# Optimization experiments

Hardware: AMD Instinct MI355X
Metric: run time of the kernel (lower is better)

Reference implementation:

```python
import jax, jax.numpy as jnp
import numpy as np

B, L, D, H = 2, 2048, 2048, 16
HD = D // H  # head_dim = 128
EPS = 1e-5


def setup_inputs() -> dict:
    key = jax.random.key(0)
    ks = jax.random.split(key, 5)
    return {
        "x": jax.random.normal(ks[0], (B, L, D), dtype=jnp.float32),
        "Wq": jax.random.normal(ks[1], (D, D), dtype=jnp.float32) * (D ** -0.5),
        "Wk": jax.random.normal(ks[2], (D, D), dtype=jnp.float32) * (D ** -0.5),
        "Wv": jax.random.normal(ks[3], (D, D), dtype=jnp.float32) * (D ** -0.5),
        "gamma_logit": jax.random.normal(ks[4], (H,), dtype=jnp.float32),
        "gn_weight": jnp.ones((D,), dtype=jnp.float32),
        "gn_bias": jnp.zeros((D,), dtype=jnp.float32),
    }


def reference(x, Wq, Wk, Wv, gamma_logit, gn_weight, gn_bias):
    scale = HD ** -0.5
    # projections (torch Linear: y = x @ W.T)
    Q = jnp.einsum('bld,ed->ble', x, Wq).reshape(B, L, H, HD).transpose(0, 2, 1, 3)
    K = jnp.einsum('bld,ed->ble', x, Wk).reshape(B, L, H, HD).transpose(0, 2, 1, 3)
    V = jnp.einsum('bld,ed->ble', x, Wv).reshape(B, L, H, HD).transpose(0, 2, 1, 3)
    # causal exponential decay matrix D[h,i,j] = gamma_h^(i-j), lower-triangular
    pos = jnp.arange(L)
    dist = jnp.abs(pos[None, :] - pos[:, None]).astype(jnp.float32)  # [L,L]
    gamma = jax.nn.sigmoid(gamma_logit)  # [H]
    Dmat = jnp.tril(gamma[:, None, None] ** dist[None, :, :])  # [H,L,L]
    # decayed linear attention (no softmax)
    attn = jnp.einsum('bhid,bhjd->bhij', Q, K) * scale * Dmat[None]
    out = jnp.einsum('bhij,bhje->bhie', attn, V)  # [B,H,L,HD]
    out = out.transpose(0, 2, 1, 3)  # [B,L,H,HD]
    # GroupNorm: channels=D, groups=H, spatial=L -> normalize per (b,h) over (L,HD)
    mean = out.mean(axis=(1, 3), keepdims=True)
    var = out.var(axis=(1, 3), keepdims=True)
    y = (out - mean) * jax.lax.rsqrt(var + EPS)
    y = y * gn_weight.reshape(1, 1, H, HD) + gn_bias.reshape(1, 1, H, HD)
    return y.reshape(B, L, D)
```

## Files before the change

kernel.cpp:

```cpp
#include <hip/hip_runtime.h>
#include <hip/hip_bf16.h>
#include <math.h>

#define B_  2
#define L_  2048
#define D_  2048
#define H_  16
#define HD_ 128
#define EPS_ 1e-5f

typedef __attribute__((ext_vector_type(8)))  short short8;
typedef __attribute__((ext_vector_type(4)))  float f32x4;
typedef __attribute__((ext_vector_type(16))) float f32x16;

static __device__ inline unsigned short bfb(float x) {
    __hip_bfloat16 h = __float2bfloat16(x);
    unsigned short s;
    __builtin_memcpy(&s, &h, 2);
    return s;
}
static __device__ inline unsigned pk2(float a, float b) {
    return (unsigned)bfb(a) | ((unsigned)bfb(b) << 16);
}

static __device__ __forceinline__ void gld_lds16(const void* g, void* l) {
    __builtin_amdgcn_global_load_lds(
        (const __attribute__((address_space(1))) unsigned int*)g,
        (__attribute__((address_space(3))) unsigned int*)l,
        16, 0, 0);
}

#define XN4 2097152
#define WN4 1048576
#define TOT4 (XN4 + 3 * WN4)

__global__ __launch_bounds__(256) void cast4_kernel(
    const float* __restrict__ x,  const float* __restrict__ Wq,
    const float* __restrict__ Wk, const float* __restrict__ Wv,
    __hip_bfloat16* __restrict__ dst)
{
    int i = blockIdx.x * 256 + threadIdx.x;
    const int st = gridDim.x * 256;
    for (; i < TOT4; i += st) {
        const float* s;
        int off;
        if (i < XN4)                { s = x;  off = i; }
        else if (i < XN4 + WN4)     { s = Wq; off = i - XN4; }
        else if (i < XN4 + 2 * WN4) { s = Wk; off = i - XN4 - WN4; }
        else                        { s = Wv; off = i - XN4 - 2 * WN4; }
        float4 v = ((const float4*)s)[off];
        uint2 r;
        r.x = pk2(v.x, v.y);
        r.y = pk2(v.z, v.w);
        ((uint2*)dst)[i] = r;
    }
}

__global__ __launch_bounds__(256) void proj_bf16(
    const __hip_bfloat16* __restrict__ X,
    const __hip_bfloat16* __restrict__ Wqb, const __hip_bfloat16* __restrict__ Wkb,
    const __hip_bfloat16* __restrict__ Wvb,
    __hip_bfloat16* __restrict__ Qo, __hip_bfloat16* __restrict__ Ko,
    __hip_bfloat16* __restrict__ Vt)
{
    const __hip_bfloat16* W = (blockIdx.z == 0) ? Wqb : (blockIdx.z == 1 ? Wkb : Wvb);
    __hip_bfloat16*       O = (blockIdx.z == 0) ? Qo  : (blockIdx.z == 1 ? Ko  : Vt);

    __shared__ __align__(16) char Al[128 * 64 * 2];
    __shared__ __align__(16) char Bl[128 * 64 * 2];

    const int t  = threadIdx.x;
    const int w  = t >> 6, l = t & 63;
    const int li = l & 15, hi4 = l >> 4;
    const int wr = w >> 1, wc = w & 1;
    const int m0 = blockIdx.y * 128;
    const int n0 = blockIdx.x * 128;

    const int srow = l >> 3;
    const int scol = ((l & 7) ^ (l >> 3)) * 8;

    f32x4 acc[4][4];
    #pragma unroll
    for (int i = 0; i < 4; ++i)
        #pragma unroll
        for (int j = 0; j < 4; ++j)
            #pragma unroll
            for (int r = 0; r < 4; ++r) acc[i][j][r] = 0.f;

    for (int k0 = 0; k0 < D_; k0 += 64) {
        if (k0) __syncthreads();
        #pragma unroll
        for (int c = 0; c < 4; ++c) {
            const int chunk = w * 4 + c;
            const int row   = chunk * 8 + srow;
            gld_lds16(X + (size_t)(m0 + row) * D_ + k0 + scol, Al + chunk * 1024);
            gld_lds16(W + (size_t)(n0 + row) * D_ + k0 + scol, Bl + chunk * 1024);
        }
        __syncthreads();

        #pragma unroll
        for (int s = 0; s < 2; ++s) {
            const int cbA = (s * 64 + hi4 * 16) ^ ((li & 7) << 4);
            short8 af[4], bf[4];
            #pragma unroll
            for (int mi = 0; mi < 4; ++mi)
                af[mi] = *(const short8*)(Al + (wr * 64 + mi * 16 + li) * 128 + cbA);
            #pragma unroll
            for (int ni = 0; ni < 4; ++ni)
                bf[ni] = *(const short8*)(Bl + (wc * 64 + ni * 16 + li) * 128 + cbA);
            #pragma unroll
            for (int mi = 0; mi < 4; ++mi)
                #pragma unroll
                for (int ni = 0; ni < 4; ++ni)
                    acc[mi][ni] = __builtin_amdgcn_mfma_f32_16x16x32_bf16(
                        af[mi], bf[ni], acc[mi][ni], 0, 0, 0);
        }
    }

    if (blockIdx.z == 2) {
        #pragma unroll
        for (int mi = 0; mi < 4; ++mi) {
            #pragma unroll
            for (int ni = 0; ni < 4; ++ni) {
                const int n     = n0 + wc * 64 + ni * 16 + li;
                const int mbase = m0 + wr * 64 + mi * 16 + hi4 * 4;
                const int b = mbase >> 11, ml = mbase & (L_ - 1);
                uint2 w2;
                w2.x = pk2(acc[mi][ni][0], acc[mi][ni][1]);
                w2.y = pk2(acc[mi][ni][2], acc[mi][ni][3]);
                *(uint2*)&O[((size_t)b * (H_ * HD_) + n) * L_ + ml] = w2;
            }
        }
    } else {
        #pragma unroll
        for (int mi = 0; mi < 4; ++mi) {
            #pragma unroll
            for (int ni = 0; ni < 4; ++ni) {
                const int n  = n0 + wc * 64 + ni * 16 + li;
                const int h  = n >> 7, hd = n & (HD_ - 1);
                #pragma unroll
                for (int r = 0; r < 4; ++r) {
                    const int m = m0 + wr * 64 + mi * 16 + hi4 * 4 + r;
                    const int b = m >> 11, ml = m & (L_ - 1);
                    O[((size_t)(b * H_ + h) * L_ + ml) * HD_ + hd] =
                        __float2bfloat16(acc[mi][ni][r]);
                }
            }
        }
    }
}

__global__ __launch_bounds__(256) void retn_kernel(
    const __hip_bfloat16* __restrict__ Qb, const __hip_bfloat16* __restrict__ Kb,
    const __hip_bfloat16* __restrict__ VT, const float* __restrict__ gl,
    float* __restrict__ out)
{
    const int bid = blockIdx.x;
    const int mm  = bid >> 5;
    const int m   = (mm < 8) ? (15 - mm) : (mm - 8);
    const int bh  = bid & 31;
    const int b   = bh >> 4, h = bh & (H_ - 1);
    const int t   = threadIdx.x;
    const int w   = t >> 6, l = t & 63;
    const int li  = l & 31, hi = l >> 5;

    const float gamma = 1.f / (1.f + __expf(-gl[h]));
    const float lg2   = __log2f(gamma);
    const float scale = 0.08838834764831845f;

    __shared__ __align__(16) char Klds[32768];
    __shared__ __align__(16) char Vlds[32768];

    const size_t base = (size_t)bh * (L_ * HD_);
    const __hip_bfloat16* VTg = VT + (size_t)bh * (HD_ * L_);
    const int i0 = m * 128 + w * 32;

    short8 qf[8];
    {
        const __hip_bfloat16* qrow = Qb + base + (size_t)(i0 + li) * HD_;
        #pragma unroll
        for (int s = 0; s < 8; ++s)
            qf[s] = *(const short8*)(qrow + s * 16 + hi * 8);
    }

    float df[16];
    #pragma unroll
    for (int r = 0; r < 16; ++r) {
        const int jl = (r & 3) + 8 * (r >> 2) + 4 * hi;
        df[r] = exp2f(lg2 * (float)(li - jl));
    }

    f32x16 acc[4];
    #pragma unroll
    for (int c = 0; c < 4; ++c)
        #pragma unroll
        for (int r = 0; r < 16; ++r) acc[c][r] = 0.f;

    const int srow4 = l >> 4;
    const int sslot = l & 15;

    for (int gj = 0; gj <= m * 128; gj += 128) {
        __syncthreads();
        #pragma unroll
        for (int cc = 0; cc < 8; ++cc) {
            const int c  = w * 8 + cc;
            const int r  = c * 4 + srow4;
            const int sc = ((sslot ^ (r & 15)) * 8);
            gld_lds16(Kb + base + (size_t)(gj + r) * HD_ + sc, Klds + c * 1024);
            gld_lds16(VTg + (size_t)r * L_ + gj + sc,          Vlds + c * 1024);
        }
        __syncthreads();

        const int tmax = ((i0 - gj) >> 5) < 3 ? ((i0 - gj) >> 5) : 3;
        for (int jt = 0; jt <= tmax; ++jt) {
            const int j0 = gj + jt * 32;

            f32x16 c;
            #pragma unroll
            for (int r = 0; r < 16; ++r) c[r] = 0.f;
            #pragma unroll
            for (int s = 0; s < 8; ++s) {
                short8 kf = *(const short8*)(Klds + (jt * 32 + li) * 256 +
                                             (((s * 2 + hi) ^ (li & 15)) << 4));
                c = __builtin_amdgcn_mfma_f32_32x32x16_bf16(kf, qf[s], c, 0, 0, 0);
            }

            float p[16];
            const float bt = exp2f(lg2 * (float)(i0 - j0)) * scale;
            if (j0 == i0) {
                #pragma unroll
                for (int r = 0; r < 16; ++r) {
                    const int jl = (r & 3) + 8 * (r >> 2) + 4 * hi;
                    p[r] = (jl <= li) ? c[r] * (df[r] * bt) : 0.f;
                }
            } else {
                #pragma unroll
                for (int r = 0; r < 16; ++r) p[r] = c[r] * (df[r] * bt);
            }

            #pragma unroll
            for (int sl = 0; sl < 2; ++sl) {
                const int o = sl * 8;
                unsigned pk01 = pk2(p[o + 0], p[o + 1]);
                unsigned pk23 = pk2(p[o + 2], p[o + 3]);
                unsigned pk45 = pk2(p[o + 4], p[o + 5]);
                unsigned pk67 = pk2(p[o + 6], p[o + 7]);
                unsigned x01 = (unsigned)__shfl_xor((int)pk01, 32);
                unsigned x23 = (unsigned)__shfl_xor((int)pk23, 32);
                unsigned x45 = (unsigned)__shfl_xor((int)pk45, 32);
                unsigned x67 = (unsigned)__shfl_xor((int)pk67, 32);
                union { short8 v; unsigned u[4]; } pf;
                pf.u[0] = hi ? x45 : pk01;
                pf.u[1] = hi ? x67 : pk23;
                pf.u[2] = hi ? pk45 : x01;
                pf.u[3] = hi ? pk67 : x23;
                #pragma unroll
                for (int cch = 0; cch < 4; ++cch) {
                    short8 vf = *(const short8*)(Vlds + (cch * 32 + li) * 256 +
                                 (((jt * 4 + sl * 2 + hi) ^ (li & 15)) << 4));
                    acc[cch] = __builtin_amdgcn_mfma_f32_32x32x16_bf16(
                        pf.v, vf, acc[cch], 0, 0, 0);
                }
            }
        }
    }

    #pragma unroll
    for (int cch = 0; cch < 4; ++cch) {
        #pragma unroll
        for (int r = 0; r < 16; ++r) {
            const int row = (r & 3) + 8 * (r >> 2) + 4 * hi;
            out[(size_t)(b * L_ + i0 + row) * D_ + h * HD_ + cch * 32 + li] =
                acc[cch][r];
        }
    }
}

__global__ __launch_bounds__(256) void gn_stats(
    const float* __restrict__ out, float2* __restrict__ part)
{
    const int bh = blockIdx.x, sl = blockIdx.y;
    const int b = bh >> 4, h = bh & (H_ - 1);
    const int t = threadIdx.x;

    float s = 0.f, sq = 0.f;
    #pragma unroll 4
    for (int it = 0; it < 16; ++it) {
        const int n  = it * 256 + t;
        const int ll = n >> 5, d4 = n & 31;
        float4 v = *(const float4*)&out[(size_t)(b * L_ + sl * 128 + ll) * D_ + h * HD_ + d4 * 4];
        s  += v.x + v.y + v.z + v.w;
        sq += v.x * v.x + v.y * v.y + v.z * v.z + v.w * v.w;
    }
    #pragma unroll
    for (int off = 32; off > 0; off >>= 1) {
        s  += __shfl_down(s, off);
        sq += __shfl_down(sq, off);
    }
    __shared__ float rs[4], rq[4];
    const int wv = t >> 6, lane = t & 63;
    if (lane == 0) { rs[wv] = s; rq[wv] = sq; }
    __syncthreads();
    if (t == 0)
        part[bh * 16 + sl] = make_float2(rs[0] + rs[1] + rs[2] + rs[3],
                                         rq[0] + rq[1] + rq[2] + rq[3]);
}

__global__ __launch_bounds__(256) void gn_apply(
    float* __restrict__ out, const float2* __restrict__ part,
    const float* __restrict__ gw, const float* __restrict__ gb)
{
    const int bh = blockIdx.x, sl = blockIdx.y;
    const int b = bh >> 4, h = bh & (H_ - 1);
    const int t = threadIdx.x;

    float S = 0.f, SQ = 0.f;
    #pragma unroll
    for (int i = 0; i < 16; ++i) {
        float2 p = part[bh * 16 + i];
        S += p.x; SQ += p.y;
    }
    const float inv  = 1.f / (float)(L_ * HD_);
    const float mean = S * inv;
    float var = SQ * inv - mean * mean;
    if (var < 0.f) var = 0.f;
    const float rstd = rsqrtf(var + EPS_);

    #pragma unroll
    for (int it = 0; it < 4; ++it) {
        const int n  = it * 256 + t;
        const int ll = n >> 5, d4 = n & 31;
        const size_t idx = (size_t)(b * L_ + sl * 32 + ll) * D_ + h * HD_ + d4 * 4;
        float4 v = *(const float4*)&out[idx];
        const float4 w4 = *(const float4*)&gw[h * HD_ + d4 * 4];
        const float4 b4 = *(const float4*)&gb[h * HD_ + d4 * 4];
        v.x = (v.x - mean) * rstd * w4.x + b4.x;
        v.y = (v.y - mean) * rstd * w4.y + b4.y;
        v.z = (v.z - mean) * rstd * w4.z + b4.z;
        v.w = (v.w - mean) * rstd * w4.w + b4.w;
        *(float4*)&out[idx] = v;
    }
}

extern "C" void kernel_launch(void* const* d_in, const int* in_sizes, int n_in,
                              void* d_out, int out_size, void* d_ws, size_t ws_size,
                              hipStream_t stream) {
    const float* x  = (const float*)d_in[0];
    const float* Wq = (const float*)d_in[1];
    const float* Wk = (const float*)d_in[2];
    const float* Wv = (const float*)d_in[3];
    const float* gl = (const float*)d_in[4];
    const float* gw = (const float*)d_in[5];
    const float* gb = (const float*)d_in[6];
    float* out = (float*)d_out;

    __hip_bfloat16* ws = (__hip_bfloat16*)d_ws;
    __hip_bfloat16* xb  = ws;
    __hip_bfloat16* Wqb = xb  + 8388608;
    __hip_bfloat16* Wkb = Wqb + 4194304;
    __hip_bfloat16* Wvb = Wkb + 4194304;
    __hip_bfloat16* Qbf = Wvb + 4194304;
    __hip_bfloat16* Kbf = Qbf + 8388608;
    __hip_bfloat16* VTb = Kbf + 8388608;
    float2* part = (float2*)(VTb + 8388608);

    cast4_kernel<<<2048, 256, 0, stream>>>(x, Wq, Wk, Wv, xb);

    dim3 pgrid(D_ / 128, (B_ * L_) / 128, 3);
    proj_bf16<<<pgrid, 256, 0, stream>>>(xb, Wqb, Wkb, Wvb, Qbf, Kbf, VTb);

    retn_kernel<<<dim3(512), 256, 0, stream>>>(Qbf, Kbf, VTb, gl, out);

    gn_stats<<<dim3(32, 16), 256, 0, stream>>>(out, part);
    gn_apply<<<dim3(32, 64), 256, 0, stream>>>(out, part, gw, gb);
}
```

Before: 224.9 us.

## Rewrite projection GEMM with 4-stage LDS pipeline, 256x128 tiles, fused QKV weights

```diff
diff --git a/kernel.cpp b/kernel.cpp
--- a/kernel.cpp
+++ b/kernel.cpp
@@ -56,28 +56,39 @@
     }
 }
 
-__global__ __launch_bounds__(256) void proj_bf16(
+#define NT_ 64
+
+__global__ __launch_bounds__(512, 2) void proj_fused(
     const __hip_bfloat16* __restrict__ X,
-    const __hip_bfloat16* __restrict__ Wqb, const __hip_bfloat16* __restrict__ Wkb,
-    const __hip_bfloat16* __restrict__ Wvb,
+    const __hip_bfloat16* __restrict__ Wc,
     __hip_bfloat16* __restrict__ Qo, __hip_bfloat16* __restrict__ Ko,
-    __hip_bfloat16* __restrict__ Vt)
+    __hip_bfloat16* __restrict__ VT)
 {
-    const __hip_bfloat16* W = (blockIdx.z == 0) ? Wqb : (blockIdx.z == 1 ? Wkb : Wvb);
-    __hip_bfloat16*       O = (blockIdx.z == 0) ? Qo  : (blockIdx.z == 1 ? Ko  : Vt);
-
-    __shared__ __align__(16) char Al[128 * 64 * 2];
-    __shared__ __align__(16) char Bl[128 * 64 * 2];
-
-    const int t  = threadIdx.x;
-    const int w  = t >> 6, l = t & 63;
-    const int li = l & 15, hi4 = l >> 4;
-    const int wr = w >> 1, wc = w & 1;
-    const int m0 = blockIdx.y * 128;
-    const int n0 = blockIdx.x * 128;
-
-    const int srow = l >> 3;
-    const int scol = ((l & 7) ^ (l >> 3)) * 8;
+    __shared__ __align__(16) char lds[98304];
+
+    const int t   = threadIdx.x;
+    const int w   = t >> 6, l = t & 63;
+    const int li  = l & 15, hi4 = l >> 4;
+    const int wr  = w >> 1, wcn = w & 1;
+
+    const int wg = ((blockIdx.x & 7) * 96) + (blockIdx.x >> 3);
+    const int m0 = (wg & 15) * 256;
+    const int n0 = (wg >> 4) * 128;
+
+    const int srow   = 16 * w + 2 * (l >> 3) + ((l & 7) >> 2);
+    const int kslot8 = ((l & 3) ^ ((l >> 3) & 3)) * 8;
+
+    const int fro  = (li >> 1) * 128 + (li & 1) * 64 + ((hi4 ^ ((li >> 1) & 3)) << 4);
+    const int aoff = wr  * 4096 + fro;
+    const int boff = wcn * 4096 + fro;
+
+    auto STAGE = [&](int tt) {
+        char* Ab = lds + (tt & 3) * 24576;
+        const size_t kc = (size_t)(tt * 32) + kslot8;
+        gld_lds16(X  + (size_t)(m0 + srow) * D_ + kc,       Ab + w * 1024);
+        gld_lds16(X  + (size_t)(m0 + 128 + srow) * D_ + kc, Ab + 8192 + w * 1024);
+        gld_lds16(Wc + (size_t)(n0 + srow) * D_ + kc,       Ab + 16384 + w * 1024);
+    };
 
     f32x4 acc[4][4];
     #pragma unroll
@@ -87,56 +98,73 @@
             #pragma unroll
             for (int r = 0; r < 4; ++r) acc[i][j][r] = 0.f;
 
-    for (int k0 = 0; k0 < D_; k0 += 64) {
-        if (k0) __syncthreads();
-        #pragma unroll
-        for (int c = 0; c < 4; ++c) {
-            const int chunk = w * 4 + c;
-            const int row   = chunk * 8 + srow;
-            gld_lds16(X + (size_t)(m0 + row) * D_ + k0 + scol, Al + chunk * 1024);
-            gld_lds16(W + (size_t)(n0 + row) * D_ + k0 + scol, Bl + chunk * 1024);
-        }
-        __syncthreads();
-
-        #pragma unroll
-        for (int s = 0; s < 2; ++s) {
-            const int cbA = (s * 64 + hi4 * 16) ^ ((li & 7) << 4);
-            short8 af[4], bf[4];
+    STAGE(0); STAGE(1); STAGE(2);
+    asm volatile("s_waitcnt vmcnt(6)" ::: "memory");
+    __builtin_amdgcn_s_barrier();
+
+    for (int tq = 0; tq < NT_ / 4; ++tq) {
+        #pragma unroll
+        for (int j = 0; j < 4; ++j) {
+            const int tt = tq * 4 + j;
+            const char* Ab = lds + j * 24576;
+            const char* Bb = Ab + 16384;
+
+            short8 af[4], bfr[4];
             #pragma unroll
             for (int mi = 0; mi < 4; ++mi)
-                af[mi] = *(const short8*)(Al + (wr * 64 + mi * 16 + li) * 128 + cbA);
+                af[mi] = *(const short8*)(Ab + aoff + mi * 1024);
             #pragma unroll
             for (int ni = 0; ni < 4; ++ni)
-                bf[ni] = *(const short8*)(Bl + (wc * 64 + ni * 16 + li) * 128 + cbA);
+                bfr[ni] = *(const short8*)(Bb + boff + ni * 1024);
+
+            if (tt <= NT_ - 4) STAGE(tt + 3);
+
+            if (tt <= NT_ - 4)      asm volatile("s_waitcnt vmcnt(6)" ::: "memory");
+            else if (tt == NT_ - 3) asm volatile("s_waitcnt vmcnt(3)" ::: "memory");
+            else if (tt == NT_ - 2) asm volatile("s_waitcnt vmcnt(0)" ::: "memory");
+
+            __builtin_amdgcn_sched_barrier(0);
+            __builtin_amdgcn_s_barrier();
+            __builtin_amdgcn_sched_barrier(0);
+
+            __builtin_amdgcn_s_setprio(1);
             #pragma unroll
             for (int mi = 0; mi < 4; ++mi)
                 #pragma unroll
                 for (int ni = 0; ni < 4; ++ni)
                     acc[mi][ni] = __builtin_amdgcn_mfma_f32_16x16x32_bf16(
-                        af[mi], bf[ni], acc[mi][ni], 0, 0, 0);
-        }
-    }
-
-    if (blockIdx.z == 2) {
+                        af[mi], bfr[ni], acc[mi][ni], 0, 0, 0);
+            __builtin_amdgcn_s_setprio(0);
+
+            __builtin_amdgcn_sched_barrier(0);
+            __builtin_amdgcn_s_barrier();
+            __builtin_amdgcn_sched_barrier(0);
+        }
+    }
+
+    const int zsel = n0 >> 11;
+    const int np   = n0 & (D_ - 1);
+    if (zsel == 2) {
         #pragma unroll
         for (int mi = 0; mi < 4; ++mi) {
             #pragma unroll
             for (int ni = 0; ni < 4; ++ni) {
-                const int n     = n0 + wc * 64 + ni * 16 + li;
+                const int n     = np + wcn * 64 + ni * 16 + li;
                 const int mbase = m0 + wr * 64 + mi * 16 + hi4 * 4;
                 const int b = mbase >> 11, ml = mbase & (L_ - 1);
                 uint2 w2;
                 w2.x = pk2(acc[mi][ni][0], acc[mi][ni][1]);
                 w2.y = pk2(acc[mi][ni][2], acc[mi][ni][3]);
-                *(uint2*)&O[((size_t)b * (H_ * HD_) + n) * L_ + ml] = w2;
+                *(uint2*)&VT[((size_t)b * D_ + n) * L_ + ml] = w2;
             }
         }
     } else {
+        __hip_bfloat16* O = zsel ? Ko : Qo;
         #pragma unroll
         for (int mi = 0; mi < 4; ++mi) {
             #pragma unroll
             for (int ni = 0; ni < 4; ++ni) {
-                const int n  = n0 + wc * 64 + ni * 16 + li;
+                const int n  = np + wcn * 64 + ni * 16 + li;
                 const int h  = n >> 7, hd = n & (HD_ - 1);
                 #pragma unroll
                 for (int r = 0; r < 4; ++r) {
@@ -366,8 +394,7 @@
 
     cast4_kernel<<<2048, 256, 0, stream>>>(x, Wq, Wk, Wv, xb);
 
-    dim3 pgrid(D_ / 128, (B_ * L_) / 128, 3);
-    proj_bf16<<<pgrid, 256, 0, stream>>>(xb, Wqb, Wkb, Wvb, Qbf, Kbf, VTb);
+    proj_fused<<<dim3(768), 512, 0, stream>>>(xb, Wqb, Qbf, Kbf, VTb);
 
     retn_kernel<<<dim3(512), 256, 0, stream>>>(Qbf, Kbf, VTb, gl, out);
 
```

Result: no change. 229.1 us (+1.9%).

## Widen projection tiles over concatenated weights and fuse GN stats into retention

Applied to the files above, without the earlier changes.

```diff
diff --git a/kernel.cpp b/kernel.cpp
--- a/kernel.cpp
+++ b/kernel.cpp
@@ -56,32 +56,30 @@
     }
 }
 
-__global__ __launch_bounds__(256) void proj_bf16(
+__global__ __launch_bounds__(256, 3) void proj_wide(
     const __hip_bfloat16* __restrict__ X,
-    const __hip_bfloat16* __restrict__ Wqb, const __hip_bfloat16* __restrict__ Wkb,
-    const __hip_bfloat16* __restrict__ Wvb,
+    const __hip_bfloat16* __restrict__ Wc,
     __hip_bfloat16* __restrict__ Qo, __hip_bfloat16* __restrict__ Ko,
-    __hip_bfloat16* __restrict__ Vt)
+    __hip_bfloat16* __restrict__ VT)
 {
-    const __hip_bfloat16* W = (blockIdx.z == 0) ? Wqb : (blockIdx.z == 1 ? Wkb : Wvb);
-    __hip_bfloat16*       O = (blockIdx.z == 0) ? Qo  : (blockIdx.z == 1 ? Ko  : Vt);
-
-    __shared__ __align__(16) char Al[128 * 64 * 2];
+    __shared__ __align__(16) char Al[256 * 64 * 2];
     __shared__ __align__(16) char Bl[128 * 64 * 2];
 
     const int t  = threadIdx.x;
     const int w  = t >> 6, l = t & 63;
     const int li = l & 15, hi4 = l >> 4;
-    const int wr = w >> 1, wc = w & 1;
-    const int m0 = blockIdx.y * 128;
-    const int n0 = blockIdx.x * 128;
+    const int wr = w >> 1, wcn = w & 1;
+
+    const int wg  = (blockIdx.x & 7) * 96 + (blockIdx.x >> 3);
+    const int m0  = (wg & 15) * 256;
+    const int n0g = (wg >> 4) * 128;
 
     const int srow = l >> 3;
     const int scol = ((l & 7) ^ (l >> 3)) * 8;
 
-    f32x4 acc[4][4];
-    #pragma unroll
-    for (int i = 0; i < 4; ++i)
+    f32x4 acc[8][4];
+    #pragma unroll
+    for (int i = 0; i < 8; ++i)
         #pragma unroll
         for (int j = 0; j < 4; ++j)
             #pragma unroll
@@ -90,57 +88,64 @@
     for (int k0 = 0; k0 < D_; k0 += 64) {
         if (k0) __syncthreads();
         #pragma unroll
-        for (int c = 0; c < 4; ++c) {
-            const int chunk = w * 4 + c;
-            const int row   = chunk * 8 + srow;
-            gld_lds16(X + (size_t)(m0 + row) * D_ + k0 + scol, Al + chunk * 1024);
-            gld_lds16(W + (size_t)(n0 + row) * D_ + k0 + scol, Bl + chunk * 1024);
+        for (int cc = 0; cc < 8; ++cc) {
+            const int c   = w * 8 + cc;
+            const int row = c * 8 + srow;
+            gld_lds16(X + (size_t)(m0 + row) * D_ + k0 + scol, Al + c * 1024);
+        }
+        #pragma unroll
+        for (int cc = 0; cc < 4; ++cc) {
+            const int c   = w * 4 + cc;
+            const int row = c * 8 + srow;
+            gld_lds16(Wc + (size_t)(n0g + row) * D_ + k0 + scol, Bl + c * 1024);
         }
         __syncthreads();
 
         #pragma unroll
         for (int s = 0; s < 2; ++s) {
-            const int cbA = (s * 64 + hi4 * 16) ^ ((li & 7) << 4);
-            short8 af[4], bf[4];
-            #pragma unroll
-            for (int mi = 0; mi < 4; ++mi)
-                af[mi] = *(const short8*)(Al + (wr * 64 + mi * 16 + li) * 128 + cbA);
+            const int cb = (s * 64 + hi4 * 16) ^ ((li & 7) << 4);
+            short8 bfr[4];
             #pragma unroll
             for (int ni = 0; ni < 4; ++ni)
-                bf[ni] = *(const short8*)(Bl + (wc * 64 + ni * 16 + li) * 128 + cbA);
-            #pragma unroll
-            for (int mi = 0; mi < 4; ++mi)
+                bfr[ni] = *(const short8*)(Bl + (wcn * 64 + ni * 16 + li) * 128 + cb);
+            #pragma unroll
+            for (int mi = 0; mi < 8; ++mi) {
+                short8 af = *(const short8*)(Al + (wr * 128 + mi * 16 + li) * 128 + cb);
                 #pragma unroll
                 for (int ni = 0; ni < 4; ++ni)
                     acc[mi][ni] = __builtin_amdgcn_mfma_f32_16x16x32_bf16(
-                        af[mi], bf[ni], acc[mi][ni], 0, 0, 0);
-        }
-    }
-
-    if (blockIdx.z == 2) {
-        #pragma unroll
-        for (int mi = 0; mi < 4; ++mi) {
+                        af, bfr[ni], acc[mi][ni], 0, 0, 0);
+            }
+        }
+    }
+
+    const int zsel = n0g >> 11;
+    const int np   = n0g & (D_ - 1);
+    if (zsel == 2) {
+        #pragma unroll
+        for (int mi = 0; mi < 8; ++mi) {
             #pragma unroll
             for (int ni = 0; ni < 4; ++ni) {
-                const int n     = n0 + wc * 64 + ni * 16 + li;
-                const int mbase = m0 + wr * 64 + mi * 16 + hi4 * 4;
+                const int n     = np + wcn * 64 + ni * 16 + li;
+                const int mbase = m0 + wr * 128 + mi * 16 + hi4 * 4;
                 const int b = mbase >> 11, ml = mbase & (L_ - 1);
                 uint2 w2;
                 w2.x = pk2(acc[mi][ni][0], acc[mi][ni][1]);
                 w2.y = pk2(acc[mi][ni][2], acc[mi][ni][3]);
-                *(uint2*)&O[((size_t)b * (H_ * HD_) + n) * L_ + ml] = w2;
+                *(uint2*)&VT[((size_t)b * D_ + n) * L_ + ml] = w2;
             }
         }
     } else {
-        #pragma unroll
-        for (int mi = 0; mi < 4; ++mi) {
+        __hip_bfloat16* O = zsel ? Ko : Qo;
+        #pragma unroll
+        for (int mi = 0; mi < 8; ++mi) {
             #pragma unroll
             for (int ni = 0; ni < 4; ++ni) {
-                const int n  = n0 + wc * 64 + ni * 16 + li;
+                const int n  = np + wcn * 64 + ni * 16 + li;
                 const int h  = n >> 7, hd = n & (HD_ - 1);
                 #pragma unroll
                 for (int r = 0; r < 4; ++r) {
-                    const int m = m0 + wr * 64 + mi * 16 + hi4 * 4 + r;
+                    const int m = m0 + wr * 128 + mi * 16 + hi4 * 4 + r;
                     const int b = m >> 11, ml = m & (L_ - 1);
                     O[((size_t)(b * H_ + h) * L_ + ml) * HD_ + hd] =
                         __float2bfloat16(acc[mi][ni][r]);
@@ -153,7 +158,7 @@
 __global__ __launch_bounds__(256) void retn_kernel(
     const __hip_bfloat16* __restrict__ Qb, const __hip_bfloat16* __restrict__ Kb,
     const __hip_bfloat16* __restrict__ VT, const float* __restrict__ gl,
-    float* __restrict__ out)
+    float* __restrict__ out, float2* __restrict__ part)
 {
     const int bid = blockIdx.x;
     const int mm  = bid >> 5;
@@ -170,6 +175,7 @@
 
     __shared__ __align__(16) char Klds[32768];
     __shared__ __align__(16) char Vlds[32768];
+    __shared__ float rs[4], rq[4];
 
     const size_t base = (size_t)bh * (L_ * HD_);
     const __hip_bfloat16* VTg = VT + (size_t)bh * (HD_ * L_);
@@ -265,45 +271,28 @@
         }
     }
 
+    float s = 0.f, sq = 0.f;
     #pragma unroll
     for (int cch = 0; cch < 4; ++cch) {
         #pragma unroll
         for (int r = 0; r < 16; ++r) {
             const int row = (r & 3) + 8 * (r >> 2) + 4 * hi;
-            out[(size_t)(b * L_ + i0 + row) * D_ + h * HD_ + cch * 32 + li] =
-                acc[cch][r];
-        }
-    }
-}
-
-__global__ __launch_bounds__(256) void gn_stats(
-    const float* __restrict__ out, float2* __restrict__ part)
-{
-    const int bh = blockIdx.x, sl = blockIdx.y;
-    const int b = bh >> 4, h = bh & (H_ - 1);
-    const int t = threadIdx.x;
-
-    float s = 0.f, sq = 0.f;
-    #pragma unroll 4
-    for (int it = 0; it < 16; ++it) {
-        const int n  = it * 256 + t;
-        const int ll = n >> 5, d4 = n & 31;
-        float4 v = *(const float4*)&out[(size_t)(b * L_ + sl * 128 + ll) * D_ + h * HD_ + d4 * 4];
-        s  += v.x + v.y + v.z + v.w;
-        sq += v.x * v.x + v.y * v.y + v.z * v.z + v.w * v.w;
-    }
+            const float v = acc[cch][r];
+            out[(size_t)(b * L_ + i0 + row) * D_ + h * HD_ + cch * 32 + li] = v;
+            s += v; sq += v * v;
+        }
+    }
+
     #pragma unroll
     for (int off = 32; off > 0; off >>= 1) {
         s  += __shfl_down(s, off);
         sq += __shfl_down(sq, off);
     }
-    __shared__ float rs[4], rq[4];
-    const int wv = t >> 6, lane = t & 63;
-    if (lane == 0) { rs[wv] = s; rq[wv] = sq; }
+    if (l == 0) { rs[w] = s; rq[w] = sq; }
     __syncthreads();
     if (t == 0)
-        part[bh * 16 + sl] = make_float2(rs[0] + rs[1] + rs[2] + rs[3],
-                                         rq[0] + rq[1] + rq[2] + rq[3]);
+        part[bh * 16 + m] = make_float2(rs[0] + rs[1] + rs[2] + rs[3],
+                                        rq[0] + rq[1] + rq[2] + rq[3]);
 }
 
 __global__ __launch_bounds__(256) void gn_apply(
@@ -366,11 +355,9 @@
 
     cast4_kernel<<<2048, 256, 0, stream>>>(x, Wq, Wk, Wv, xb);
 
-    dim3 pgrid(D_ / 128, (B_ * L_) / 128, 3);
-    proj_bf16<<<pgrid, 256, 0, stream>>>(xb, Wqb, Wkb, Wvb, Qbf, Kbf, VTb);
-
-    retn_kernel<<<dim3(512), 256, 0, stream>>>(Qbf, Kbf, VTb, gl, out);
-
-    gn_stats<<<dim3(32, 16), 256, 0, stream>>>(out, part);
+    proj_wide<<<dim3(768), 256, 0, stream>>>(xb, Wqb, Qbf, Kbf, VTb);
+
+    retn_kernel<<<dim3(512), 256, 0, stream>>>(Qbf, Kbf, VTb, gl, out, part);
+
     gn_apply<<<dim3(32, 64), 256, 0, stream>>>(out, part, gw, gb);
 }
```

Result: slower. 359.5 us (+59.9%).
